# Optimization experiments

Hardware: AMD Instinct MI355X
Metric: run time of the kernel (lower is better)

The kernel has to match this reference:

```python
import jax, jax.numpy as jnp
import numpy as np
import math

C = 96; HEADS = 3; HD = C // HEADS; WS = 8; B = 4; H = 256; W = 256
EPS = 1e-5; SCALE = HD ** -0.5; LOGIT_MAX = math.log(1.0 / 0.01)
N = WS * WS


def _rel_pos():
    coords = np.stack(np.meshgrid(np.arange(WS), np.arange(WS), indexing='ij')).reshape(2, -1)
    rel = (coords[:, :, None] - coords[:, None, :]).transpose(1, 2, 0).astype(np.float32)
    return jnp.asarray(np.sign(rel) * np.log1p(np.abs(rel)))  # [N, N, 2]

REL = _rel_pos()


def conv1x1(x, w, b):
    return jnp.einsum('bchw,oc->bohw', x, w) + b[None, :, None, None]


def dwconv(x, w, b, pad, reflect=False):
    if reflect:
        x = jnp.pad(x, ((0, 0), (0, 0), (pad, pad), (pad, pad)), mode='reflect')
        padding = 'VALID'
    else:
        padding = [(pad, pad), (pad, pad)]
    y = jax.lax.conv_general_dilated(x, w, (1, 1), padding,
                                     feature_group_count=x.shape[1],
                                     dimension_numbers=('NCHW', 'OIHW', 'NCHW'))
    return y + b[None, :, None, None]


def window_partition(x):  # [B,H,W,C] -> [nW, WS*WS, C]
    b, h, w, c = x.shape
    x = x.reshape(b, h // WS, WS, w // WS, WS, c).transpose(0, 1, 3, 2, 4, 5)
    return x.reshape(-1, WS * WS, c)


def window_reverse(win, h, w):  # [nW, WS*WS, C] -> [B,H,W,C]
    b = win.shape[0] // ((h // WS) * (w // WS))
    x = win.reshape(b, h // WS, w // WS, WS, WS, -1).transpose(0, 1, 3, 2, 4, 5)
    return x.reshape(b, h, w, -1)


def setup_inputs() -> dict:
    key = jax.random.key(0)
    ks = jax.random.split(key, 16)
    def nrm(k, shape, std=0.02):
        return jax.random.normal(k, shape, jnp.float32) * std
    inp = {'x': jax.random.normal(ks[0], (B, C, H, W), jnp.float32)}
    inp.update(
        agn_weight=jnp.ones((C,), jnp.float32), agn_bias=jnp.zeros((C,), jnp.float32),
        meta1_w=nrm(ks[1], (C,)), meta1_b=jnp.ones((C,), jnp.float32),
        meta2_w=nrm(ks[2], (C,)), meta2_b=jnp.zeros((C,), jnp.float32),
        la1_w=nrm(ks[3], (C, 1, 3, 3)), la1_b=jnp.zeros((C,), jnp.float32),
        la2_w=nrm(ks[4], (C, 1, 3, 3)), la2_b=jnp.zeros((C,), jnp.float32),
        ta1_w=nrm(ks[5], (C, 1, 3, 3)), ta1_b=jnp.zeros((C,), jnp.float32),
        ta2_w=nrm(ks[6], (C, 1, 3, 3)), ta2_b=jnp.zeros((C,), jnp.float32),
        q_w=nrm(ks[7], (C, C)), q_b=jnp.zeros((C,), jnp.float32),
        kv_w=nrm(ks[8], (2 * C, C)), kv_b=jnp.zeros((2 * C,), jnp.float32),
        dw_w=nrm(ks[9], (C, 1, 5, 5)), dw_b=jnp.zeros((C,), jnp.float32),
        proj_w=nrm(ks[10], (C, C)), proj_b=jnp.zeros((C,), jnp.float32),
        logit_scale=jnp.asarray(math.log(1.0 / 0.07), jnp.float32),
        rp_w1=nrm(ks[11], (256, 2)), rp_b1=jnp.zeros((256,), jnp.float32),
        rp_w2=nrm(ks[12], (HEADS, 256)), rp_b2=jnp.zeros((HEADS,), jnp.float32),
        m1_w=nrm(ks[13], (4 * C, C)), m1_b=jnp.zeros((4 * C,), jnp.float32),
        m2_w=nrm(ks[14], (C, 4 * C)), m2_b=jnp.zeros((C,), jnp.float32),
    )
    return inp


def reference(x, agn_weight, agn_bias, meta1_w, meta1_b, meta2_w, meta2_b,
              la1_w, la1_b, la2_w, la2_b, ta1_w, ta1_b, ta2_w, ta2_b,
              q_w, q_b, kv_w, kv_b, dw_w, dw_b, proj_w, proj_b,
              logit_scale, rp_w1, rp_b1, rp_w2, rp_b2,
              m1_w, m1_b, m2_w, m2_b):
    identity = x
    # ---- AGN: per-sample global mean/std norm + dynamic affine + two dw-conv branches
    mean = jnp.mean(x, axis=(1, 2, 3), keepdims=True)                      # [B,1,1,1]
    std = jnp.sqrt(jnp.mean((x - mean) ** 2, axis=(1, 2, 3), keepdims=True) + EPS)
    xn = (x - mean) / std
    rescale = std * meta1_w[None, :, None, None] + meta1_b[None, :, None, None]   # conv1x1(1->C) on std
    rebias = mean * meta2_w[None, :, None, None] + meta2_b[None, :, None, None]
    local = dwconv(jax.nn.relu(dwconv(xn, la1_w, la1_b, 1)), la2_w, la2_b, 1)
    texture = dwconv(jax.nn.relu(dwconv(xn, ta1_w, ta1_b, 1)), ta2_w, ta2_b, 1)
    xn = xn * (agn_weight[None, :, None, None] * rescale) + (agn_bias[None, :, None, None] + rebias) + local + texture
    # ---- DSAttention (use_attn, DWConv, shift_size=0, H%WS==0 so no padding)
    Q = conv1x1(xn, q_w, q_b)
    KV = conv1x1(xn, kv_w, kv_b)                                           # [B,2C,H,W]
    qkv_img = jnp.concatenate([Q, KV], axis=1).transpose(0, 2, 3, 1)       # [B,H,W,3C]
    co = dwconv(Q, dw_w, dw_b, 2, reflect=True).transpose(0, 2, 3, 1)      # reflect-padded 5x5 dwconv
    qkv = window_partition(qkv_img)                                        # [nW,N,3C]
    cw = window_partition(co)                                              # [nW,N,C]
    nW = qkv.shape[0]
    qkv = qkv.reshape(nW, N, 3, HEADS, HD).transpose(2, 0, 3, 1, 4)        # [3,nW,h,N,hd]
    q = cw.reshape(nW, N, HEADS, HD).transpose(0, 2, 1, 3)                 # q replaced by conv branch
    k = qkv[1] * SCALE
    v = qkv[2]
    ls = jnp.exp(jnp.minimum(logit_scale, LOGIT_MAX))
    hb = jax.nn.relu(REL @ rp_w1.T + rp_b1)                                # [N,N,256]
    bias = (hb @ rp_w2.T + rp_b2).transpose(2, 0, 1)                       # [h,N,N]
    attn = jax.nn.softmax(jnp.einsum('whnd,whmd->whnm', q, k) * ls + bias[None], axis=-1)
    o = jnp.einsum('whnm,whmd->whnd', attn, v).transpose(0, 2, 1, 3).reshape(nW, N, C)
    out = window_reverse(o, x.shape[2], x.shape[3]).transpose(0, 3, 1, 2)  # [B,C,H,W]
    a = conv1x1(out, proj_w, proj_b)
    x = identity + a * rescale + rebias
    # ---- MLP (1x1 conv -> ReLU -> 1x1 conv), residual
    x = x + conv1x1(jax.nn.relu(conv1x1(x, m1_w, m1_b)), m2_w, m2_b)
    return x
```

## Files before the change

### kernel.cpp

```cpp
#include <hip/hip_runtime.h>
#include <hip/hip_bf16.h>

typedef __hip_bfloat16 bf16;

#define PER_B     6291456
#define EPS_F     1e-5f
#define SCALE_F   0.17677669529663687f
#define LOGIT_MAX_F 4.605170185988092f

__device__ __forceinline__ float b2f(bf16 v){ return __bfloat162float(v); }
__device__ __forceinline__ bf16  f2b(float v){ return __float2bfloat16(v); }

template<int DT> __device__ __forceinline__ float rdf(const void* p, size_t i){
  return DT ? ((const float*)p)[i] : b2f(((const bf16*)p)[i]);
}
template<int DT> __device__ __forceinline__ void wrf(void* p, size_t i, float v){
  if (DT) ((float*)p)[i] = v; else ((bf16*)p)[i] = f2b(v);
}
template<int DT> __device__ __forceinline__ float2 rd2(const void* p, size_t i){
  if (DT) return *(const float2*)((const float*)p + i);
  unsigned u = *(const unsigned*)((const bf16*)p + i);
  return make_float2(__uint_as_float(u << 16), __uint_as_float(u & 0xffff0000u));
}

typedef __attribute__((ext_vector_type(8))) short short8v;
typedef __attribute__((ext_vector_type(4))) short short4v;
typedef __attribute__((ext_vector_type(4))) float f32x4;

__device__ __forceinline__ short f2bs(float v){
  unsigned u = __float_as_uint(v);
  return (short)((u + 0x7fffu + ((u >> 16) & 1u)) >> 16);
}
__device__ __forceinline__ float bs2f(short s){
  return __uint_as_float(((unsigned)(unsigned short)s) << 16);
}

template<int DT> __device__ __forceinline__ short8v ld8(const void* p, size_t i){
  short8v a;
  if (DT){
    const float* f = (const float*)p + i;
    float4 lo = *(const float4*)f;
    float4 hi = *(const float4*)(f + 4);
    a[0]=f2bs(lo.x); a[1]=f2bs(lo.y); a[2]=f2bs(lo.z); a[3]=f2bs(lo.w);
    a[4]=f2bs(hi.x); a[5]=f2bs(hi.y); a[6]=f2bs(hi.z); a[7]=f2bs(hi.w);
  } else {
    a = *(const short8v*)((const short*)p + i);
  }
  return a;
}
template<int DT> __device__ __forceinline__ short8v ld4x2(const void* p, size_t i0){
  short8v a;
  if (DT){
    const float* f = (const float*)p;
    float4 lo = *(const float4*)(f + i0);
    float4 hi = *(const float4*)(f + i0 + 16);
    a[0]=f2bs(lo.x); a[1]=f2bs(lo.y); a[2]=f2bs(lo.z); a[3]=f2bs(lo.w);
    a[4]=f2bs(hi.x); a[5]=f2bs(hi.y); a[6]=f2bs(hi.z); a[7]=f2bs(hi.w);
  } else {
    const short* s = (const short*)p;
    short4v lo = *(const short4v*)(s + i0);
    short4v hi = *(const short4v*)(s + i0 + 16);
    a[0]=lo[0]; a[1]=lo[1]; a[2]=lo[2]; a[3]=lo[3];
    a[4]=hi[0]; a[5]=hi[1]; a[6]=hi[2]; a[7]=hi[3];
  }
  return a;
}

__global__ __launch_bounds__(256) void k_detect(const void* __restrict__ x, int* __restrict__ flag){
  __shared__ int cnt;
  if (threadIdx.x == 0) cnt = 0;
  __syncthreads();
  float v = b2f(((const bf16*)x)[(size_t)threadIdx.x * 16]);
  int bad = (!(v == v)) || (fabsf(v) > 1e20f);
  if (bad) atomicAdd(&cnt, 1);
  __syncthreads();
  if (threadIdx.x == 0) *flag = (cnt >= 4) ? 1 : 0;
}

template<int DT>
__global__ __launch_bounds__(256) void k_stats_partial(const void* __restrict__ x,
    float* __restrict__ partials, const int* __restrict__ flag){
  if (*flag != DT) return;
  int blk = blockIdx.x;
  int b = blk >> 8, chunk = blk & 255;
  const int chunkN = PER_B / 256;
  size_t base = (size_t)b * PER_B + (size_t)chunk * chunkN;
  float s = 0.f, ss = 0.f;
  for (int i = threadIdx.x; i < chunkN; i += 256){
    float v = rdf<DT>(x, base + i); s += v; ss += v*v;
  }
  __shared__ float sh[512];
  sh[threadIdx.x] = s; sh[256 + threadIdx.x] = ss;
  __syncthreads();
  for (int st = 128; st > 0; st >>= 1){
    if (threadIdx.x < st){
      sh[threadIdx.x]     += sh[threadIdx.x + st];
      sh[256+threadIdx.x] += sh[256+threadIdx.x + st];
    }
    __syncthreads();
  }
  if (threadIdx.x == 0){ partials[blk*2] = sh[0]; partials[blk*2+1] = sh[256]; }
}

template<int DT>
__global__ __launch_bounds__(256) void k_stats_final(const float* __restrict__ partials,
    const void* m1w, const void* m1b, const void* m2w, const void* m2b,
    float* __restrict__ stats, const int* __restrict__ flag){
  if (*flag != DT) return;
  __shared__ float sh[512];
  __shared__ float mS[4], sS[4];
  for (int b = 0; b < 4; b++){
    sh[threadIdx.x]     = partials[(b*256+threadIdx.x)*2];
    sh[256+threadIdx.x] = partials[(b*256+threadIdx.x)*2+1];
    __syncthreads();
    for (int st = 128; st > 0; st >>= 1){
      if (threadIdx.x < st){
        sh[threadIdx.x]     += sh[threadIdx.x + st];
        sh[256+threadIdx.x] += sh[256+threadIdx.x + st];
      }
      __syncthreads();
    }
    if (threadIdx.x == 0){
      float mean = sh[0] / (float)PER_B;
      float var  = sh[256] / (float)PER_B - mean*mean;
      float stdv = sqrtf(var + EPS_F);
      mS[b] = mean; sS[b] = stdv;
      stats[b] = mean; stats[4+b] = stdv;
    }
    __syncthreads();
  }
  for (int t = threadIdx.x; t < 384; t += 256){
    int b = t / 96, c = t % 96;
    stats[8+t]   = sS[b]*rdf<DT>(m1w,c) + rdf<DT>(m1b,c);
    stats[392+t] = mS[b]*rdf<DT>(m2w,c) + rdf<DT>(m2b,c);
  }
}

template<int DT>
__global__ __launch_bounds__(256) void k_bias(const void* w1, const void* b1v,
    const void* w2, const void* b2v, float* __restrict__ biasT, const int* __restrict__ flag){
  if (*flag != DT) return;
  int i = blockIdx.x >> 6, j = blockIdx.x & 63;
  int dy = (i>>3) - (j>>3), dx = (i&7) - (j&7);
  float fy = (float)dy, fx = (float)dx;
  float r0 = copysignf(log1pf(fabsf(fy)), fy);
  float r1 = copysignf(log1pf(fabsf(fx)), fx);
  int t = threadIdx.x;
  float hb = fmaxf(r0*rdf<DT>(w1,t*2) + r1*rdf<DT>(w1,t*2+1) + rdf<DT>(b1v,t), 0.f);
  __shared__ float sh[256];
  for (int h = 0; h < 3; h++){
    sh[t] = hb * rdf<DT>(w2, h*256+t);
    __syncthreads();
    for (int st = 128; st > 0; st >>= 1){ if (t < st) sh[t] += sh[t+st]; __syncthreads(); }
    if (t == 0) biasT[h*4096 + j*64 + i] = sh[0] + rdf<DT>(b2v, h);
    __syncthreads();
  }
}

template<int DT>
__global__ __launch_bounds__(256) void k_agn_fused(const void* __restrict__ x,
    const float* __restrict__ stats,
    const void* la1w, const void* la1b, const void* la2w, const void* la2b,
    const void* ta1w, const void* ta1b, const void* ta2w, const void* ta2b,
    const void* agnw, const void* agnb,
    bf16* __restrict__ xn2, const int* __restrict__ flag){
  if (*flag != DT) return;
  __shared__ float xs[400];
  __shared__ float ts[324];
  __shared__ float us[324];
  int idx = blockIdx.x;
  int tile = idx & 255; int bc = idx >> 8; int c = bc % 96; int b = bc / 96;
  int oy = (tile >> 4) << 4, ox = (tile & 15) << 4;
  float mean = stats[b], sd = stats[4+b];
  size_t xbase = ((size_t)bc) << 16;
  for (int it = threadIdx.x; it < 400; it += 256){
    int ly = it / 20, lx = it % 20;
    int gy = oy - 2 + ly, gx = ox - 2 + lx;
    float v = 0.f;
    if (gy >= 0 && gy < 256 && gx >= 0 && gx < 256)
      v = (rdf<DT>(x, xbase + (gy<<8) + gx) - mean) / sd;
    xs[it] = v;
  }
  float wl1[9], wt1[9], wl2[9], wt2[9];
  #pragma unroll
  for (int k = 0; k < 9; k++){
    wl1[k] = rdf<DT>(la1w, c*9+k); wt1[k] = rdf<DT>(ta1w, c*9+k);
    wl2[k] = rdf<DT>(la2w, c*9+k); wt2[k] = rdf<DT>(ta2w, c*9+k);
  }
  float bl1 = rdf<DT>(la1b, c), bt1 = rdf<DT>(ta1b, c);
  __syncthreads();
  for (int it = threadIdx.x; it < 324; it += 256){
    int ly = it / 18, lx = it % 18;
    int cy = oy - 1 + ly, cx = ox - 1 + lx;
    float a1 = 0.f, a2 = 0.f;
    if (cy >= 0 && cy < 256 && cx >= 0 && cx < 256){
      a1 = bl1; a2 = bt1;
      #pragma unroll
      for (int dy = 0; dy < 3; dy++)
        #pragma unroll
        for (int dx = 0; dx < 3; dx++){
          float v = xs[(ly+dy)*20 + lx+dx];
          a1 += v * wl1[dy*3+dx]; a2 += v * wt1[dy*3+dx];
        }
      a1 = fmaxf(a1, 0.f); a2 = fmaxf(a2, 0.f);
    }
    ts[it] = a1; us[it] = a2;
  }
  __syncthreads();
  int ty = threadIdx.x >> 4, tx0 = threadIdx.x & 15;
  float l = rdf<DT>(la2b, c), t = rdf<DT>(ta2b, c);
  #pragma unroll
  for (int dy = 0; dy < 3; dy++)
    #pragma unroll
    for (int dx = 0; dx < 3; dx++){
      l += ts[(ty+dy)*18 + tx0+dx] * wl2[dy*3+dx];
      t += us[(ty+dy)*18 + tx0+dx] * wt2[dy*3+dx];
    }
  float v = xs[(ty+2)*20 + tx0+2];
  float r = v*(rdf<DT>(agnw,c)*stats[8+bc]) + (rdf<DT>(agnb,c) + stats[392+bc]) + l + t;
  xn2[xbase + ((oy+ty)<<8) + ox + tx0] = f2b(r);
}

#define CS_OFF 0
#define XS_OFF 13312
#define QB_OFF 43264
#define KT_OFF 13312
#define VD_OFF 26624
#define XC_OFF 40448
#define PS_OFF 40448
#define OS_OFF 13312

template<int DT>
__global__ __launch_bounds__(256, 3) void k_attn_mega(const bf16* __restrict__ xn2,
    const void* qw, const void* qb, const void* kvw, const void* kvb,
    const void* dww, const void* dwb, const void* pw, const void* pb,
    const void* lsin, const float* __restrict__ biasT,
    const void* __restrict__ xin, const float* __restrict__ stats,
    void* __restrict__ outp, const int* __restrict__ flag){
  if (*flag != DT) return;
  __shared__ __align__(16) char smem[53760];
  int tid = threadIdx.x, wid = blockIdx.x;
  int b = wid >> 10, wy = (wid >> 5) & 31, wx = wid & 31;
  int wv = tid >> 6, ln = tid & 63;
  int r = ln & 15, q = ln >> 4;

  {
    short* xs = (short*)(smem + XS_OFF);
    for (int it = tid; it < 13824; it += 256){
      int t = it % 144, craw = it / 144;
      int c = craw ^ ((t >> 3) & 7);
      int ty = (wy<<3) - 2 + t/12, tx = (wx<<3) - 2 + t%12;
      ty = ty < 0 ? -ty : (ty > 255 ? 510 - ty : ty);
      tx = tx < 0 ? -tx : (tx > 255 ? 510 - tx : tx);
      xs[t*104 + c] = ((const short*)xn2)[(((size_t)(b*96 + c))<<16) + (ty<<8) + tx];
    }
  }
  __syncthreads();

  {
    const short* xs = (const short*)(smem + XS_OFF);
    short* Qb = (short*)(smem + QB_OFF) + wv*1184;
    short* cs = (short*)(smem + CS_OFF);
    int ty0 = (ln>>3)+2, tx0 = (ln&7)+2;
    for (int mt = wv; mt < 6; mt += 4){
      short8v aw[3];
      #pragma unroll
      for (int kt = 0; kt < 3; kt++)
        aw[kt] = ld8<DT>(qw, (size_t)(16*mt + r)*96 + 32*kt + 8*q);
      float qb4[4];
      #pragma unroll
      for (int j = 0; j < 4; j++) qb4[j] = rdf<DT>(qb, 16*mt + 4*q + j);
      float accs[9][4];
      #pragma unroll
      for (int nt = 0; nt < 9; nt++){
        f32x4 acc = {0.f,0.f,0.f,0.f};
        #pragma unroll
        for (int kt = 0; kt < 3; kt++){
          short8v bx = *(const short8v*)(xs + (16*nt + r)*104 + 32*kt + 8*q);
          acc = __builtin_amdgcn_mfma_f32_16x16x32_bf16(aw[kt], bx, acc, 0, 0, 0);
        }
        #pragma unroll
        for (int j = 0; j < 4; j++) accs[nt][j] = acc[j] + qb4[j];
      }
      if (q < 2){
        #pragma unroll
        for (int nt = 0; nt < 9; nt++)
          #pragma unroll
          for (int j = 0; j < 4; j++)
            Qb[(4*q+j)*148 + 16*nt + r] = f2bs(accs[nt][j]);
      }
      asm volatile("s_waitcnt lgkmcnt(0)" ::: "memory");
      for (int cl = 0; cl < 8; cl++){
        int c = 16*mt + cl;
        float a = rdf<DT>(dwb, c);
        #pragma unroll
        for (int dy = -2; dy <= 2; dy++)
          #pragma unroll
          for (int dx = -2; dx <= 2; dx++)
            a += bs2f(Qb[cl*148 + (ty0+dy)*12 + tx0+dx]) * rdf<DT>(dww, c*25 + (dy+2)*5 + dx+2);
        cs[ln*104 + c] = f2bs(a);
      }
      asm volatile("s_waitcnt lgkmcnt(0)" ::: "memory");
      if (q >= 2){
        #pragma unroll
        for (int nt = 0; nt < 9; nt++)
          #pragma unroll
          for (int j = 0; j < 4; j++)
            Qb[(4*(q-2)+j)*148 + 16*nt + r] = f2bs(accs[nt][j]);
      }
      asm volatile("s_waitcnt lgkmcnt(0)" ::: "memory");
      for (int cl = 8; cl < 16; cl++){
        int c = 16*mt + cl;
        float a = rdf<DT>(dwb, c);
        #pragma unroll
        for (int dy = -2; dy <= 2; dy++)
          #pragma unroll
          for (int dx = -2; dx <= 2; dx++)
            a += bs2f(Qb[(cl-8)*148 + (ty0+dy)*12 + tx0+dx]) * rdf<DT>(dww, c*25 + (dy+2)*5 + dx+2);
        cs[ln*104 + c] = f2bs(a);
      }
      asm volatile("s_waitcnt lgkmcnt(0)" ::: "memory");
    }
  }
  __syncthreads();

  {
    short* xc = (short*)(smem + XC_OFF);
    for (int it = tid; it < 768; it += 256){
      int c = it >> 3, row = it & 7;
      const short* src = (const short*)xn2 + (((size_t)(b*96 + c))<<16)
                         + (((wy<<3)+row)<<8) + (wx<<3);
      short8v v = *(const short8v*)src;
      #pragma unroll
      for (int k = 0; k < 8; k++){
        int pe = k ^ row;
        xc[(row*8+pe)*104 + c] = v[pe];
      }
    }
  }
  __syncthreads();
  {
    const short* xc = (const short*)(smem + XC_OFF);
    short* Kt = (short*)(smem + KT_OFF);
    short* Vd = (short*)(smem + VD_OFF);
    for (int mtk = wv; mtk < 12; mtk += 4){
      short8v aw[3];
      #pragma unroll
      for (int kt = 0; kt < 3; kt++)
        aw[kt] = ld8<DT>(kvw, (size_t)(16*mtk + r)*96 + 32*kt + 8*q);
      float bb[4];
      #pragma unroll
      for (int j = 0; j < 4; j++) bb[j] = rdf<DT>(kvb, 16*mtk + 4*q + j);
      for (int nt = 0; nt < 4; nt++){
        f32x4 acc = {0.f,0.f,0.f,0.f};
        #pragma unroll
        for (int kt = 0; kt < 3; kt++){
          short8v bx = *(const short8v*)(xc + (16*nt + r)*104 + 32*kt + 8*q);
          acc = __builtin_amdgcn_mfma_f32_16x16x32_bf16(aw[kt], bx, acc, 0, 0, 0);
        }
        if (mtk < 6){
          short4v kv;
          #pragma unroll
          for (int j = 0; j < 4; j++) kv[j] = f2bs((acc[j] + bb[j]) * SCALE_F);
          *(short4v*)(Kt + (16*nt + r)*104 + 16*mtk + 4*q) = kv;
        } else {
          #pragma unroll
          for (int j = 0; j < 4; j++)
            Vd[(16*(mtk-6) + 4*q + j)*72 + 16*nt + r] = f2bs(acc[j] + bb[j]);
        }
      }
    }
  }
  __syncthreads();

  float o_save[24];
  {
    const short* cs = (const short*)(smem + CS_OFF);
    const short* Kt = (const short*)(smem + KT_OFF);
    const short* Vd = (const short*)(smem + VD_OFF);
    short* Psw = (short*)(smem + PS_OFF) + wv*1152;
    float lsv = __expf(fminf(rdf<DT>(lsin, 0), LOGIT_MAX_F));
    #pragma unroll
    for (int h = 0; h < 3; h++){
      short8v qa = *(const short8v*)(cs + (16*wv + r)*104 + 32*h + 8*q);
      f32x4 s[4];
      #pragma unroll
      for (int mt = 0; mt < 4; mt++){
        short8v kb = *(const short8v*)(Kt + (16*mt + r)*104 + 32*h + 8*q);
        f32x4 z = {0.f,0.f,0.f,0.f};
        s[mt] = __builtin_amdgcn_mfma_f32_16x16x32_bf16(qa, kb, z, 0, 0, 0);
      }
      float l[4][4];
      #pragma unroll
      for (int mt = 0; mt < 4; mt++){
        float4 bv = *(const float4*)(biasT + h*4096 + (16*mt + r)*64 + 16*wv + 4*q);
        l[mt][0] = s[mt][0]*lsv + bv.x;
        l[mt][1] = s[mt][1]*lsv + bv.y;
        l[mt][2] = s[mt][2]*lsv + bv.z;
        l[mt][3] = s[mt][3]*lsv + bv.w;
      }
      float mx[4], sm[4];
      #pragma unroll
      for (int j = 0; j < 4; j++){
        float m0 = fmaxf(fmaxf(l[0][j], l[1][j]), fmaxf(l[2][j], l[3][j]));
        m0 = fmaxf(m0, __shfl_xor(m0, 1));
        m0 = fmaxf(m0, __shfl_xor(m0, 2));
        m0 = fmaxf(m0, __shfl_xor(m0, 4));
        m0 = fmaxf(m0, __shfl_xor(m0, 8));
        mx[j] = m0; sm[j] = 0.f;
      }
      #pragma unroll
      for (int mt = 0; mt < 4; mt++)
        #pragma unroll
        for (int j = 0; j < 4; j++){
          float p = __expf(l[mt][j] - mx[j]);
          sm[j] += p;
          Psw[(4*q+j)*72 + 16*mt + r] = f2bs(p);
        }
      #pragma unroll
      for (int j = 0; j < 4; j++){
        sm[j] += __shfl_xor(sm[j], 1);
        sm[j] += __shfl_xor(sm[j], 2);
        sm[j] += __shfl_xor(sm[j], 4);
        sm[j] += __shfl_xor(sm[j], 8);
      }
      float inv[4];
      #pragma unroll
      for (int j = 0; j < 4; j++) inv[j] = 1.f / sm[j];
      asm volatile("s_waitcnt lgkmcnt(0)" ::: "memory");
      short8v pa0 = *(const short8v*)(Psw + r*72 + 8*q);
      short8v pa1 = *(const short8v*)(Psw + r*72 + 32 + 8*q);
      #pragma unroll
      for (int dt = 0; dt < 2; dt++){
        f32x4 o = {0.f,0.f,0.f,0.f};
        short8v vb0 = *(const short8v*)(Vd + (32*h + 16*dt + r)*72 + 8*q);
        short8v vb1 = *(const short8v*)(Vd + (32*h + 16*dt + r)*72 + 32 + 8*q);
        o = __builtin_amdgcn_mfma_f32_16x16x32_bf16(pa0, vb0, o, 0, 0, 0);
        o = __builtin_amdgcn_mfma_f32_16x16x32_bf16(pa1, vb1, o, 0, 0, 0);
        #pragma unroll
        for (int j = 0; j < 4; j++) o_save[h*8 + dt*4 + j] = o[j] * inv[j];
      }
      asm volatile("s_waitcnt lgkmcnt(0)" ::: "memory");
    }
  }
  __syncthreads();

  {
    short* os = (short*)(smem + OS_OFF);
    #pragma unroll
    for (int h = 0; h < 3; h++)
      #pragma unroll
      for (int dt = 0; dt < 2; dt++)
        #pragma unroll
        for (int j = 0; j < 4; j++)
          os[(16*wv + 4*q + j)*104 + 32*h + 16*dt + r] = f2bs(o_save[h*8 + dt*4 + j]);
  }
  __syncthreads();

  {
    const short* os = (const short*)(smem + OS_OFF);
    short8v ob[3];
    #pragma unroll
    for (int kt = 0; kt < 3; kt++)
      ob[kt] = *(const short8v*)(os + (16*wv + r)*104 + 32*kt + 8*q);
    for (int mt = 0; mt < 6; mt++){
      f32x4 acc = {0.f,0.f,0.f,0.f};
      #pragma unroll
      for (int kt = 0; kt < 3; kt++){
        short8v aw = ld8<DT>(pw, (size_t)(16*mt + r)*96 + 32*kt + 8*q);
        acc = __builtin_amdgcn_mfma_f32_16x16x32_bf16(aw, ob[kt], acc, 0, 0, 0);
      }
      #pragma unroll
      for (int j = 0; j < 4; j++){
        int oc = 16*mt + 4*q + j;
        int n  = 16*wv + r;
        int gy = (wy<<3) + (n>>3), gx = (wx<<3) + (n&7);
        size_t gi = (((size_t)(b*96 + oc))<<16) + (gy<<8) + gx;
        float a = acc[j] + rdf<DT>(pb, oc);
        float x1 = rdf<DT>(xin, gi) + a*stats[8 + b*96 + oc] + stats[392 + b*96 + oc];
        wrf<DT>(outp, gi, x1);
      }
    }
  }
}

template<int DT>
__global__ __launch_bounds__(256) void k_mlp_mfma(void* __restrict__ io,
    const void* w1, const void* b1, const void* w2, const void* b2v,
    const int* __restrict__ flag){
  if (*flag != DT) return;
  __shared__ __align__(16) short x1s[256*104];
  int blk = blockIdx.x; int b = blk >> 8; int pix0 = (blk & 255) << 8;
  int tid = threadIdx.x;

  for (int c = 0; c < 96; c++){
    size_t gi = (((size_t)(b*96 + c))<<16) + pix0 + tid;
    short v = DT ? f2bs(((const float*)io)[gi]) : ((const short*)io)[gi];
    x1s[tid*104 + c] = v;
  }
  __syncthreads();

  int wv = tid >> 6, l = tid & 63;
  int r = l & 15, q = l >> 4;
  int pbase = wv << 6;

  f32x4 acc2[6][4];
  #pragma unroll
  for (int mt = 0; mt < 6; mt++)
    #pragma unroll
    for (int nt = 0; nt < 4; nt++)
      acc2[mt][nt] = (f32x4){0.f,0.f,0.f,0.f};

  #pragma unroll 2
  for (int t = 0; t < 12; t++){
    short8v aA[3], aB[3];
    #pragma unroll
    for (int kt = 0; kt < 3; kt++){
      aA[kt] = ld8<DT>(w1, (size_t)(32*t + r)*96      + 32*kt + 8*q);
      aB[kt] = ld8<DT>(w1, (size_t)(32*t + 16 + r)*96 + 32*kt + 8*q);
    }
    float bA[4], bB[4];
    #pragma unroll
    for (int j = 0; j < 4; j++){
      bA[j] = rdf<DT>(b1, 32*t + 4*q + j);
      bB[j] = rdf<DT>(b1, 32*t + 16 + 4*q + j);
    }
    f32x4 a1A[4], a1B[4];
    #pragma unroll
    for (int nt = 0; nt < 4; nt++){
      a1A[nt] = (f32x4){0.f,0.f,0.f,0.f};
      a1B[nt] = (f32x4){0.f,0.f,0.f,0.f};
    }
    #pragma unroll
    for (int kt = 0; kt < 3; kt++){
      #pragma unroll
      for (int nt = 0; nt < 4; nt++){
        short8v bx = *(const short8v*)&x1s[(pbase + 16*nt + r)*104 + 32*kt + 8*q];
        a1A[nt] = __builtin_amdgcn_mfma_f32_16x16x32_bf16(aA[kt], bx, a1A[nt], 0, 0, 0);
        a1B[nt] = __builtin_amdgcn_mfma_f32_16x16x32_bf16(aB[kt], bx, a1B[nt], 0, 0, 0);
      }
    }
    short8v B2[4];
    #pragma unroll
    for (int nt = 0; nt < 4; nt++){
      short8v h;
      #pragma unroll
      for (int j = 0; j < 4; j++){
        h[j]   = f2bs(fmaxf(a1A[nt][j] + bA[j], 0.f));
        h[4+j] = f2bs(fmaxf(a1B[nt][j] + bB[j], 0.f));
      }
      B2[nt] = h;
    }
    #pragma unroll
    for (int mt = 0; mt < 6; mt++){
      short8v wA = ld4x2<DT>(w2, (size_t)(16*mt + r)*384 + 32*t + 4*q);
      #pragma unroll
      for (int nt = 0; nt < 4; nt++)
        acc2[mt][nt] = __builtin_amdgcn_mfma_f32_16x16x32_bf16(wA, B2[nt], acc2[mt][nt], 0, 0, 0);
    }
  }

  #pragma unroll
  for (int mt = 0; mt < 6; mt++)
    #pragma unroll
    for (int nt = 0; nt < 4; nt++)
      #pragma unroll
      for (int j = 0; j < 4; j++){
        int oc = 16*mt + 4*q + j;
        int pl = pbase + 16*nt + r;
        size_t gi = (((size_t)(b*96 + oc))<<16) + pix0 + pl;
        float v = acc2[mt][nt][j] + rdf<DT>(b2v, oc);
        if (DT){
          ((float*)io)[gi] = ((const float*)io)[gi] + v;
        } else {
          ((bf16*)io)[gi] = f2b(bs2f(x1s[pl*104 + oc]) + v);
        }
      }
}

extern "C" void kernel_launch(void* const* d_in, const int* in_sizes, int n_in,
                              void* d_out, int out_size, void* d_ws, size_t ws_size,
                              hipStream_t stream) {
  const void* x      = d_in[0];
  const void* agnw   = d_in[1];
  const void* agnb   = d_in[2];
  const void* meta1w = d_in[3];
  const void* meta1b = d_in[4];
  const void* meta2w = d_in[5];
  const void* meta2b = d_in[6];
  const void* la1w   = d_in[7];
  const void* la1b   = d_in[8];
  const void* la2w   = d_in[9];
  const void* la2b   = d_in[10];
  const void* ta1w   = d_in[11];
  const void* ta1b   = d_in[12];
  const void* ta2w   = d_in[13];
  const void* ta2b   = d_in[14];
  const void* qw     = d_in[15];
  const void* qb     = d_in[16];
  const void* kvw    = d_in[17];
  const void* kvb    = d_in[18];
  const void* dww    = d_in[19];
  const void* dwb    = d_in[20];
  const void* pw     = d_in[21];
  const void* pb     = d_in[22];
  const void* lsin   = d_in[23];
  const void* rpw1   = d_in[24];
  const void* rpb1   = d_in[25];
  const void* rpw2   = d_in[26];
  const void* rpb2   = d_in[27];
  const void* m1w    = d_in[28];
  const void* m1b    = d_in[29];
  const void* m2w    = d_in[30];
  const void* m2b    = d_in[31];

  char* ws = (char*)d_ws;
  int*   flag     = (int*)ws;
  float* partials = (float*)(ws + 256);
  float* stats    = (float*)(ws + 8448);
  float* biasT    = (float*)(ws + 12288);
  bf16*  xn2      = (bf16*)(ws + 65536);

  k_detect<<<1, 256, 0, stream>>>(x, flag);

  k_stats_partial<0><<<1024, 256, 0, stream>>>(x, partials, flag);
  k_stats_final<0>  <<<1,    256, 0, stream>>>(partials, meta1w, meta1b, meta2w, meta2b, stats, flag);
  k_bias<0>         <<<4096, 256, 0, stream>>>(rpw1, rpb1, rpw2, rpb2, biasT, flag);
  k_agn_fused<0>    <<<98304,256, 0, stream>>>(x, stats, la1w, la1b, la2w, la2b,
                                               ta1w, ta1b, ta2w, ta2b, agnw, agnb, xn2, flag);
  k_attn_mega<0>    <<<4096, 256, 0, stream>>>(xn2, qw, qb, kvw, kvb, dww, dwb, pw, pb,
                                               lsin, biasT, x, stats, d_out, flag);
  k_mlp_mfma<0>     <<<1024, 256, 0, stream>>>(d_out, m1w, m1b, m2w, m2b, flag);

  k_stats_partial<1><<<1024, 256, 0, stream>>>(x, partials, flag);
  k_stats_final<1>  <<<1,    256, 0, stream>>>(partials, meta1w, meta1b, meta2w, meta2b, stats, flag);
  k_bias<1>         <<<4096, 256, 0, stream>>>(rpw1, rpb1, rpw2, rpb2, biasT, flag);
  k_agn_fused<1>    <<<98304,256, 0, stream>>>(x, stats, la1w, la1b, la2w, la2b,
                                               ta1w, ta1b, ta2w, ta2b, agnw, agnb, xn2, flag);
  k_attn_mega<1>    <<<4096, 256, 0, stream>>>(xn2, qw, qb, kvw, kvb, dww, dwb, pw, pb,
                                               lsin, biasT, x, stats, d_out, flag);
  k_mlp_mfma<1>     <<<1024, 256, 0, stream>>>(d_out, m1w, m1b, m2w, m2b, flag);
}
```

Measured before the change: 1.107 ms.

## Vectorize halo load, swizzle block order, and make dwconv staging channel-contiguous

Interior windows now load their 12x12 halo tile row by row with 16-byte vector loads instead of scattered 2-byte gathers. Border windows keep the reflect-padding gather. The Q-projection staging buffer becomes position-major with 8 channels contiguous, so the 5x5 depthwise conv reads one short8 per tap and writes its 8 outputs in one vector store. Block indices are permuted so that consecutive blocks map to windows spread across the image, which changes L2 locality. Interior halo tiles are stored without the XOR channel swizzle the fallback path uses, so the MFMA reads of that buffer may hit more LDS bank conflicts.

```diff
diff --git a/kernel.cpp b/kernel.cpp
--- a/kernel.cpp
+++ b/kernel.cpp
@@ -239,27 +239,46 @@
     void* __restrict__ outp, const int* __restrict__ flag){
   if (*flag != DT) return;
   __shared__ __align__(16) char smem[53760];
-  int tid = threadIdx.x, wid = blockIdx.x;
+  int tid = threadIdx.x;
+  int wid = ((blockIdx.x & 7) << 9) | (blockIdx.x >> 3);
   int b = wid >> 10, wy = (wid >> 5) & 31, wx = wid & 31;
   int wv = tid >> 6, ln = tid & 63;
   int r = ln & 15, q = ln >> 4;
 
   {
     short* xs = (short*)(smem + XS_OFF);
-    for (int it = tid; it < 13824; it += 256){
-      int t = it % 144, craw = it / 144;
-      int c = craw ^ ((t >> 3) & 7);
-      int ty = (wy<<3) - 2 + t/12, tx = (wx<<3) - 2 + t%12;
-      ty = ty < 0 ? -ty : (ty > 255 ? 510 - ty : ty);
-      tx = tx < 0 ? -tx : (tx > 255 ? 510 - tx : tx);
-      xs[t*104 + c] = ((const short*)xn2)[(((size_t)(b*96 + c))<<16) + (ty<<8) + tx];
+    bool interior = (wy >= 1 && wy <= 30 && wx >= 1 && wx <= 30);
+    if (interior){
+      const short* xb = (const short*)xn2;
+      for (int it = tid; it < 1152; it += 256){
+        int c = it / 12, row = it % 12;
+        int gy = (wy<<3) - 2 + row;
+        const short* src = xb + (((size_t)(b*96 + c))<<16) + (gy<<8) + (wx<<3);
+        short8v L = *(const short8v*)(src - 8);
+        short8v M = *(const short8v*)(src);
+        short8v R = *(const short8v*)(src + 8);
+        short* dst = xs + (row*12)*104 + c;
+        dst[0*104]  = L[6]; dst[1*104]  = L[7];
+        #pragma unroll
+        for (int k = 0; k < 8; k++) dst[(2+k)*104] = M[k];
+        dst[10*104] = R[0]; dst[11*104] = R[1];
+      }
+    } else {
+      for (int it = tid; it < 13824; it += 256){
+        int t = it % 144, craw = it / 144;
+        int c = craw ^ ((t >> 3) & 7);
+        int ty = (wy<<3) - 2 + t/12, tx = (wx<<3) - 2 + t%12;
+        ty = ty < 0 ? -ty : (ty > 255 ? 510 - ty : ty);
+        tx = tx < 0 ? -tx : (tx > 255 ? 510 - tx : tx);
+        xs[t*104 + c] = ((const short*)xn2)[(((size_t)(b*96 + c))<<16) + (ty<<8) + tx];
+      }
     }
   }
   __syncthreads();
 
   {
     const short* xs = (const short*)(smem + XS_OFF);
-    short* Qb = (short*)(smem + QB_OFF) + wv*1184;
+    short* Qb = (short*)(smem + QB_OFF) + wv*1152;
     short* cs = (short*)(smem + CS_OFF);
     int ty0 = (ln>>3)+2, tx0 = (ln&7)+2;
     for (int mt = wv; mt < 6; mt += 4){
@@ -282,44 +301,36 @@
         #pragma unroll
         for (int j = 0; j < 4; j++) accs[nt][j] = acc[j] + qb4[j];
       }
-      if (q < 2){
-        #pragma unroll
-        for (int nt = 0; nt < 9; nt++)
+      #pragma unroll
+      for (int hf = 0; hf < 2; hf++){
+        if ((q >> 1) == hf){
+          int cl = 4*(q & 1);
           #pragma unroll
-          for (int j = 0; j < 4; j++)
-            Qb[(4*q+j)*148 + 16*nt + r] = f2bs(accs[nt][j]);
-      }
-      asm volatile("s_waitcnt lgkmcnt(0)" ::: "memory");
-      for (int cl = 0; cl < 8; cl++){
-        int c = 16*mt + cl;
-        float a = rdf<DT>(dwb, c);
+          for (int nt = 0; nt < 9; nt++)
+            #pragma unroll
+            for (int j = 0; j < 4; j++)
+              Qb[(16*nt + r)*8 + cl + j] = f2bs(accs[nt][j]);
+        }
+        asm volatile("s_waitcnt lgkmcnt(0)" ::: "memory");
+        float acc8[8];
+        #pragma unroll
+        for (int k = 0; k < 8; k++) acc8[k] = rdf<DT>(dwb, 16*mt + 8*hf + k);
         #pragma unroll
         for (int dy = -2; dy <= 2; dy++)
           #pragma unroll
-          for (int dx = -2; dx <= 2; dx++)
-            a += bs2f(Qb[cl*148 + (ty0+dy)*12 + tx0+dx]) * rdf<DT>(dww, c*25 + (dy+2)*5 + dx+2);
-        cs[ln*104 + c] = f2bs(a);
-      }
-      asm volatile("s_waitcnt lgkmcnt(0)" ::: "memory");
-      if (q >= 2){
-        #pragma unroll
-        for (int nt = 0; nt < 9; nt++)
-          #pragma unroll
-          for (int j = 0; j < 4; j++)
-            Qb[(4*(q-2)+j)*148 + 16*nt + r] = f2bs(accs[nt][j]);
-      }
-      asm volatile("s_waitcnt lgkmcnt(0)" ::: "memory");
-      for (int cl = 8; cl < 16; cl++){
-        int c = 16*mt + cl;
-        float a = rdf<DT>(dwb, c);
-        #pragma unroll
-        for (int dy = -2; dy <= 2; dy++)
-          #pragma unroll
-          for (int dx = -2; dx <= 2; dx++)
-            a += bs2f(Qb[(cl-8)*148 + (ty0+dy)*12 + tx0+dx]) * rdf<DT>(dww, c*25 + (dy+2)*5 + dx+2);
-        cs[ln*104 + c] = f2bs(a);
-      }
-      asm volatile("s_waitcnt lgkmcnt(0)" ::: "memory");
+          for (int dx = -2; dx <= 2; dx++){
+            int pos = (ty0+dy)*12 + tx0+dx;
+            short8v v = *(const short8v*)(Qb + pos*8);
+            #pragma unroll
+            for (int k = 0; k < 8; k++)
+              acc8[k] += bs2f(v[k]) * rdf<DT>(dww, (16*mt + 8*hf + k)*25 + (dy+2)*5 + dx+2);
+          }
+        short8v outv;
+        #pragma unroll
+        for (int k = 0; k < 8; k++) outv[k] = f2bs(acc8[k]);
+        *(short8v*)(cs + ln*104 + 16*mt + 8*hf) = outv;
+        asm volatile("s_waitcnt lgkmcnt(0)" ::: "memory");
+      }
     }
   }
   __syncthreads();
```

Measured after the change: 1.152 ms. 1.04x slower.
